# Optimization experiments

Hardware: AMD Instinct MI355X
Metric: run time of the kernel (lower is better)

## Reference

```python
import jax, jax.numpy as jnp
import numpy as np

N = 50000
E = 1600000
IN_C = 512
HID = 128
HEADS = 8
OUT_C = 64
NEG_SLOPE = 0.2


def setup_inputs() -> dict:
    key = jax.random.key(0)
    ks = jax.random.split(key, 10)
    x = jax.random.normal(ks[0], (N, IN_C), dtype=jnp.float32)
    edge_index = jax.random.randint(ks[1], (2, E), 0, N, dtype=jnp.int32)
    s1 = 1.0 / np.sqrt(IN_C)
    W1 = jax.random.uniform(ks[2], (IN_C, HEADS * HID), jnp.float32, -s1, s1)
    att_src1 = jax.random.normal(ks[3], (HEADS, HID), jnp.float32) * 0.1
    att_dst1 = jax.random.normal(ks[4], (HEADS, HID), jnp.float32) * 0.1
    b1 = jnp.zeros((HEADS * HID,), jnp.float32)
    s2 = 1.0 / np.sqrt(HEADS * HID)
    W2 = jax.random.uniform(ks[5], (HEADS * HID, OUT_C), jnp.float32, -s2, s2)
    att_src2 = jax.random.normal(ks[6], (1, OUT_C), jnp.float32) * 0.1
    att_dst2 = jax.random.normal(ks[7], (1, OUT_C), jnp.float32) * 0.1
    b2 = jnp.zeros((OUT_C,), jnp.float32)
    return {"x": x, "edge_index": edge_index, "W1": W1, "att_src1": att_src1,
            "att_dst1": att_dst1, "b1": b1, "W2": W2, "att_src2": att_src2,
            "att_dst2": att_dst2, "b2": b2}


def gat_conv(x, src, dst, W, a_src, a_dst, b, heads, ch, concat):
    n = x.shape[0]
    h = (x @ W).reshape(n, heads, ch)                      # [N,H,C]
    alpha_s = jnp.einsum('nhc,hc->nh', h, a_src)           # [N,H]
    alpha_d = jnp.einsum('nhc,hc->nh', h, a_dst)           # [N,H]
    logits = jax.nn.leaky_relu(alpha_s[src] + alpha_d[dst], NEG_SLOPE)  # [E,H]
    # segment softmax over edges grouped by destination node
    m = jax.ops.segment_max(logits, dst, num_segments=n)
    e = jnp.exp(logits - m[dst])
    z = jax.ops.segment_sum(e, dst, num_segments=n)
    alpha = e / z[dst]                                     # [E,H]
    msg = h[src] * alpha[:, :, None]                       # [E,H,C]
    out = jax.ops.segment_sum(msg, dst, num_segments=n)    # [N,H,C]
    out = out.reshape(n, heads * ch) if concat else out.mean(axis=1)
    return out + b


def reference(x, edge_index, W1, att_src1, att_dst1, b1, W2, att_src2, att_dst2, b2):
    n = x.shape[0]
    loops = jnp.arange(n, dtype=edge_index.dtype)
    src = jnp.concatenate([edge_index[0], loops])
    dst = jnp.concatenate([edge_index[1], loops])
    h = gat_conv(x, src, dst, W1, att_src1, att_dst1, b1, HEADS, HID, True)
    h = jax.nn.elu(h)
    out = gat_conv(h, src, dst, W2, att_src2, att_dst2, b2, 1, OUT_C, False)
    return jax.nn.log_softmax(out, axis=1)
```

## Files before the change

kernel.cpp:

```cpp
#include <hip/hip_runtime.h>
#include <hip/hip_bf16.h>

#define NN 50000
#define EE 1600000
#define ET (EE + NN)
#define HEADS 8
#define HID 128
#define INC 512
#define H1C (HEADS * HID)
#define OUTC 64
#define NEG_SLOPE 0.2f

typedef unsigned short u16;
typedef unsigned int u32;
typedef unsigned char u8;
typedef __attribute__((ext_vector_type(8))) __bf16 bf16x8;
typedef __attribute__((ext_vector_type(4))) float f32x4;
typedef __attribute__((ext_vector_type(2))) float f32x2;
typedef __attribute__((ext_vector_type(4))) u32 u32x4;

__device__ __forceinline__ float lrelu(float x) { return x > 0.f ? x : NEG_SLOPE * x; }
__device__ __forceinline__ float us2f(u16 u) { return __uint_as_float(((u32)u) << 16); }
__device__ __forceinline__ u16 f2bs(float f) {
    u32 u = __float_as_uint(f);
    u += 0x7fffu + ((u >> 16) & 1u);
    return (u16)(u >> 16);
}

__device__ __forceinline__ void gload_lds16(const void* g, void* lds) {
    __builtin_amdgcn_global_load_lds((const __attribute__((address_space(1))) void*)g,
                                     (__attribute__((address_space(3))) void*)lds, 16, 0, 0);
}

__global__ __launch_bounds__(256) void cvt_x_k(const float* __restrict__ x, u16* __restrict__ xb) {
    int i = blockIdx.x * 256 + threadIdx.x;
    float4 v = ((const float4*)x)[i];
    ushort4 o; o.x = f2bs(v.x); o.y = f2bs(v.y); o.z = f2bs(v.z); o.w = f2bs(v.w);
    ((ushort4*)xb)[i] = o;
}

__global__ __launch_bounds__(256) void cvt_w1t_k(const float* __restrict__ W, u16* __restrict__ Wt) {
    int idx = blockIdx.x * 256 + threadIdx.x;
    int n = idx >> 9, k = idx & 511;
    Wt[idx] = f2bs(W[k * 1024 + n]);
}

__global__ __launch_bounds__(256) void cvt_w2t_k(const float* __restrict__ W, u16* __restrict__ Wt) {
    int idx = blockIdx.x * 256 + threadIdx.x;
    int n = idx >> 10, k = idx & 1023;
    Wt[idx] = f2bs(W[k * 64 + n]);
}

__global__ __launch_bounds__(256) void hist_k(const int* __restrict__ ei, int* __restrict__ cnt) {
    int e = blockIdx.x * 256 + threadIdx.x;
    if (e >= ET) return;
    int d = (e < EE) ? ei[EE + e] : (e - EE);
    atomicAdd(&cnt[d], 1);
}

__global__ __launch_bounds__(256) void scan1_k(const int* __restrict__ cnt,
                                               int* __restrict__ startp, int* __restrict__ bsum) {
    __shared__ int ws[8];
    int tid = threadIdx.x;
    int i = blockIdx.x * 256 + tid;
    int v = (i < NN) ? cnt[i] : 0;
    int lane = tid & 63, w = tid >> 6;
    int x = v;
#pragma unroll
    for (int off = 1; off < 64; off <<= 1) { int t = __shfl_up(x, off); if (lane >= off) x += t; }
    if (lane == 63) ws[w] = x;
    __syncthreads();
    if (tid == 0) { int s = 0; for (int k = 0; k < 4; ++k) { int t = ws[k]; ws[k] = s; s += t; } }
    __syncthreads();
    x += ws[w];
    if (i < NN) startp[i] = x - v;
    if (tid == 255) bsum[blockIdx.x] = x;
}

__global__ __launch_bounds__(256) void scan2_k(const int* __restrict__ bsum,
                                               int* __restrict__ boff, int nb) {
    __shared__ int ws[8];
    int tid = threadIdx.x;
    int v = (tid < nb) ? bsum[tid] : 0;
    int lane = tid & 63, w = tid >> 6;
    int x = v;
#pragma unroll
    for (int off = 1; off < 64; off <<= 1) { int t = __shfl_up(x, off); if (lane >= off) x += t; }
    if (lane == 63) ws[w] = x;
    __syncthreads();
    if (tid == 0) { int s = 0; for (int k = 0; k < 4; ++k) { int t = ws[k]; ws[k] = s; s += t; } }
    __syncthreads();
    x += ws[w];
    if (tid < nb) boff[tid] = x - v;
}

__global__ __launch_bounds__(256) void scan3_k(int* __restrict__ startp, const int* __restrict__ boff) {
    int i = blockIdx.x * 256 + threadIdx.x;
    if (i < NN) startp[i] += boff[blockIdx.x];
}

__global__ __launch_bounds__(256) void scatter_k(const int* __restrict__ ei,
                                                 const int* __restrict__ start,
                                                 int* __restrict__ cursor,
                                                 int* __restrict__ csr_src) {
    int e = blockIdx.x * 256 + threadIdx.x;
    if (e >= ET) return;
    int s, d;
    if (e < EE) { s = ei[e]; d = ei[EE + e]; }
    else        { s = e - EE; d = e - EE; }
    int pos = start[d] + atomicAdd(&cursor[d], 1);
    csr_src[pos] = s;
}

__device__ __forceinline__ void stf(float* p, float v) { *p = v; }
__device__ __forceinline__ void stf(u16* p, float v)   { *p = f2bs(v); }
__device__ __forceinline__ void stf(u8* p, float v) {
    u32 pk = __builtin_amdgcn_cvt_pk_fp8_f32(v, v, 0, false);
    *p = (u8)(pk & 0xff);
}

template<int BM, int BN, typename TC, bool FUSE, int SWZ>
__global__ __launch_bounds__(256) void mgemm_k(const u16* __restrict__ A,
                                               const u16* __restrict__ Bt,
                                               TC* __restrict__ C,
                                               const float* __restrict__ att_s,
                                               const float* __restrict__ att_d,
                                               float* __restrict__ as_o,
                                               float* __restrict__ ad_o,
                                               int M, int K, int Ncol, int NH) {
    __shared__ __align__(16) u16 As[BM * 64];
    __shared__ __align__(16) u16 Bs[BN * 64];
    __shared__ float asL[2][BM], adL[2][BM];
    int tid = threadIdx.x;
    int wid = tid >> 6, lane = tid & 63;

    int wg = blockIdx.x;
    if (SWZ) { int q = gridDim.x >> 3; wg = (blockIdx.x & 7) * q + (blockIdx.x >> 3); }
    int nbn = Ncol / BN;
    int bm_i = wg / nbn, bn_i = wg % nbn;
    int bm = bm_i * BM, bn = bn_i * BN;

    constexpr int WN = BN / 2;
    constexpr int FM = 4;
    constexpr int FN = WN / 16;
    constexpr int TA = BM * 64 * 2 / 1024;
    constexpr int TB = BN * 64 * 2 / 1024;
    int wr = wid >> 1, wc = wid & 1;

    f32x4 acc[FM][FN] = {};

    for (int k0 = 0; k0 < K; k0 += 64) {
#pragma unroll
        for (int i = 0; i < TA / 4; ++i) {
            int t = wid * (TA / 4) + i;
            int o = t * 1024 + lane * 16;
            int m = o >> 7;
            int b = o & 127;
            int kb = b ^ ((m & 7) << 4);
            int gm = bm + m; if (gm >= M) gm = M - 1;
            gload_lds16(A + ((size_t)gm * K + k0 + (kb >> 1)), (char*)As + t * 1024);
        }
#pragma unroll
        for (int i = 0; i < TB / 4; ++i) {
            int t = wid * (TB / 4) + i;
            int o = t * 1024 + lane * 16;
            int n = o >> 7;
            int b = o & 127;
            int kb = b ^ ((n & 7) << 4);
            gload_lds16(Bt + ((size_t)(bn + n) * K + k0 + (kb >> 1)), (char*)Bs + t * 1024);
        }
        __syncthreads();
        int g = lane >> 4, r = lane & 15;
#pragma unroll
        for (int kh = 0; kh < 2; ++kh) {
            int kbb = g * 16 + kh * 64;
            bf16x8 af[FM], bfr[FN];
#pragma unroll
            for (int fm = 0; fm < FM; ++fm) {
                int m = wr * 64 + fm * 16 + r;
                af[fm] = *(const bf16x8*)((const char*)As + m * 128 + (kbb ^ ((m & 7) << 4)));
            }
#pragma unroll
            for (int fn = 0; fn < FN; ++fn) {
                int n = wc * WN + fn * 16 + r;
                bfr[fn] = *(const bf16x8*)((const char*)Bs + n * 128 + (kbb ^ ((n & 7) << 4)));
            }
#pragma unroll
            for (int fm = 0; fm < FM; ++fm)
#pragma unroll
                for (int fn = 0; fn < FN; ++fn)
                    acc[fm][fn] = __builtin_amdgcn_mfma_f32_16x16x32_bf16(af[fm], bfr[fn], acc[fm][fn], 0, 0, 0);
        }
        __syncthreads();
    }
#pragma unroll
    for (int fm = 0; fm < FM; ++fm)
#pragma unroll
        for (int fn = 0; fn < FN; ++fn)
#pragma unroll
            for (int rr = 0; rr < 4; ++rr) {
                int gm = bm + wr * 64 + fm * 16 + (lane >> 4) * 4 + rr;
                int gn = bn + wc * WN + fn * 16 + (lane & 15);
                if (gm < M) stf(&C[(size_t)gm * Ncol + gn], acc[fm][fn][rr]);
            }

    if constexpr (FUSE) {
        float asv[FN], adv[FN];
#pragma unroll
        for (int fn = 0; fn < FN; ++fn) {
            int c = bn + wc * WN + fn * 16 + (lane & 15);
            asv[fn] = att_s[c]; adv[fn] = att_d[c];
        }
#pragma unroll
        for (int fm = 0; fm < FM; ++fm)
#pragma unroll
            for (int rr = 0; rr < 4; ++rr) {
                float ps = 0.f, pd = 0.f;
#pragma unroll
                for (int fn = 0; fn < FN; ++fn) {
                    ps += acc[fm][fn][rr] * asv[fn];
                    pd += acc[fm][fn][rr] * adv[fn];
                }
#pragma unroll
                for (int off = 1; off < 16; off <<= 1) {
                    ps += __shfl_xor(ps, off);
                    pd += __shfl_xor(pd, off);
                }
                if ((lane & 15) == 0) {
                    int rl = wr * 64 + fm * 16 + (lane >> 4) * 4 + rr;
                    asL[wc][rl] = ps; adL[wc][rl] = pd;
                }
            }
        __syncthreads();
        if (tid < BM) {
            int gm = bm + tid;
            if (gm < M) {
                as_o[(size_t)gm * NH + bn_i] = asL[0][tid] + asL[1][tid];
                ad_o[(size_t)gm * NH + bn_i] = adL[0][tid] + adL[1][tid];
            }
        }
    }
}

__global__ __launch_bounds__(256) void agg1_k(const u8* __restrict__ h1,
                                              const float* __restrict__ as1,
                                              const float* __restrict__ ad1,
                                              const int* __restrict__ start,
                                              const int* __restrict__ cnt,
                                              const int* __restrict__ csr_src,
                                              const float* __restrict__ b1,
                                              u16* __restrict__ out1) {
    int n = blockIdx.x;
    int tid = threadIdx.x;
    int s0 = start[n], deg = cnt[n];
    __shared__ float ad_sh[8], rz_sh[8];
    __shared__ int src_sh[64];
    __shared__ float al_sh[64][8];
    __shared__ float zred[256];
    __shared__ float comb[3][64][17];

    if (tid < 8) ad_sh[tid] = ad1[n * 8 + tid];
    __syncthreads();

    int l = tid & 63, grp = tid >> 6;
    int myh = l >> 3;
    float acc[16] = {};
    float zacc = 0.f;
    const char* h1b = (const char*)h1;

    for (int e0 = 0; e0 < deg; e0 += 64) {
        int ne = min(64, deg - e0);
        if (tid < ne) src_sh[tid] = csr_src[s0 + e0 + tid];
        __syncthreads();
        for (int i = tid; i < ne * 8; i += 256) {
            int ee = i >> 3, hh = i & 7;
            int s = src_sh[ee];
            float al = __expf(lrelu(as1[s * 8 + hh] + ad_sh[hh]));
            al_sh[ee][hh] = al;
            zacc += al;
        }
        __syncthreads();
        int j = grp;
        if (j < ne) {
            u32x4 v = *(const u32x4*)(h1b + (size_t)src_sh[j] * 1024 + l * 16);
            while (true) {
                int jn = j + 4;
                bool more = jn < ne;
                u32x4 vn;
                if (more) vn = *(const u32x4*)(h1b + (size_t)src_sh[jn] * 1024 + l * 16);
                float al = al_sh[j][myh];
#pragma unroll
                for (int w = 0; w < 4; ++w) {
                    u32 word = v[w];
                    f32x2 p0 = __builtin_amdgcn_cvt_pk_f32_fp8(word, false);
                    f32x2 p1 = __builtin_amdgcn_cvt_pk_f32_fp8(word, true);
                    acc[w * 4 + 0] += al * p0.x;
                    acc[w * 4 + 1] += al * p0.y;
                    acc[w * 4 + 2] += al * p1.x;
                    acc[w * 4 + 3] += al * p1.y;
                }
                if (!more) break;
                v = vn; j = jn;
            }
        }
        __syncthreads();
    }

    zred[tid] = zacc;
    __syncthreads();
#pragma unroll
    for (int off = 128; off >= 8; off >>= 1) {
        if (tid < off) zred[tid] += zred[tid + off];
        __syncthreads();
    }
    if (tid < 8) rz_sh[tid] = 1.f / zred[tid];
    __syncthreads();

    if (grp) {
#pragma unroll
        for (int c = 0; c < 16; ++c) comb[grp - 1][l][c] = acc[c];
    }
    __syncthreads();
    if (!grp) {
        float rz = rz_sh[myh];
        int cbase = l * 16;
        float o[16];
#pragma unroll
        for (int c = 0; c < 16; ++c) {
            float zz = (acc[c] + comb[0][l][c] + comb[1][l][c] + comb[2][l][c]) * rz + b1[cbase + c];
            o[c] = zz > 0.f ? zz : (__expf(zz) - 1.f);
        }
        u32x4 pk0, pk1;
#pragma unroll
        for (int i = 0; i < 4; ++i) {
            pk0[i] = (u32)f2bs(o[2 * i])     | ((u32)f2bs(o[2 * i + 1]) << 16);
            pk1[i] = (u32)f2bs(o[8 + 2 * i]) | ((u32)f2bs(o[9 + 2 * i]) << 16);
        }
        char* dst = (char*)out1 + (size_t)n * 2048 + l * 32;
        __builtin_nontemporal_store(pk0, (u32x4*)dst);
        __builtin_nontemporal_store(pk1, (u32x4*)(dst + 16));
    }
}

__global__ __launch_bounds__(256) void agg2_k(const u16* __restrict__ h2,
                                              const float* __restrict__ as2,
                                              const float* __restrict__ ad2,
                                              const int* __restrict__ start,
                                              const int* __restrict__ cnt,
                                              const int* __restrict__ csr_src,
                                              const float* __restrict__ b2,
                                              float* __restrict__ out) {
    int n = blockIdx.x * 4 + (threadIdx.x >> 6);
    int lane = threadIdx.x & 63;
    if (n >= NN) return;
    int s0 = start[n], deg = cnt[n];
    float adn = ad2[n];

    int half = lane >> 5, l = lane & 31;
    float a0 = 0.f, a1 = 0.f, z = 0.f;
    int j = half;
    if (j < deg) {
        int s = csr_src[s0 + j];
        float asv = as2[s];
        u32 v = *(const u32*)(h2 + (size_t)s * 64 + l * 2);
        while (true) {
            int jn = j + 2;
            bool more = jn < deg;
            int sn; float asn; u32 vn;
            if (more) {
                sn = csr_src[s0 + jn];
                asn = as2[sn];
                vn = *(const u32*)(h2 + (size_t)sn * 64 + l * 2);
            }
            float al = __expf(lrelu(asv + adn));
            z += al;
            a0 += al * us2f((u16)(v & 0xffff));
            a1 += al * us2f((u16)(v >> 16));
            if (!more) break;
            asv = asn; v = vn; j = jn;
        }
    }
    a0 += __shfl_xor(a0, 32);
    a1 += __shfl_xor(a1, 32);
    z  += __shfl_xor(z, 32);
    float rz = 1.f / z;
    float y0 = a0 * rz + b2[2 * l], y1 = a1 * rz + b2[2 * l + 1];

    float mm = fmaxf(y0, y1);
#pragma unroll
    for (int off = 16; off; off >>= 1) mm = fmaxf(mm, __shfl_xor(mm, off));
    float se = __expf(y0 - mm) + __expf(y1 - mm);
#pragma unroll
    for (int off = 16; off; off >>= 1) se += __shfl_xor(se, off);
    float ls = __logf(se);
    if (half == 0) {
        float2 o; o.x = y0 - mm - ls; o.y = y1 - mm - ls;
        *(float2*)(out + (size_t)n * 64 + 2 * l) = o;
    }
}

extern "C" void kernel_launch(void* const* d_in, const int* in_sizes, int n_in,
                              void* d_out, int out_size, void* d_ws, size_t ws_size,
                              hipStream_t stream) {
    const float* x     = (const float*)d_in[0];
    const int*   ei    = (const int*)d_in[1];
    const float* W1    = (const float*)d_in[2];
    const float* aw_s1 = (const float*)d_in[3];
    const float* aw_d1 = (const float*)d_in[4];
    const float* b1    = (const float*)d_in[5];
    const float* W2    = (const float*)d_in[6];
    const float* aw_s2 = (const float*)d_in[7];
    const float* aw_d2 = (const float*)d_in[8];
    const float* b2    = (const float*)d_in[9];
    float* out = (float*)d_out;

    char* ws = (char*)d_ws;
    size_t off = 0;
    auto alloc = [&](size_t bytes) -> void* {
        void* p = (void*)(ws + off);
        off += (bytes + 511) & ~(size_t)511;
        return p;
    };
    u16*   out1    = (u16*)alloc((size_t)NN * H1C * 2);
    u16*   xb      = out1;
    u8*    h1      = (u8*)alloc((size_t)NN * H1C);
    u16*   h2      = (u16*)h1;
    u16*   w1t     = (u16*)alloc((size_t)H1C * INC * 2);
    u16*   w2t     = (u16*)alloc((size_t)OUTC * H1C * 2);
    float* as1     = (float*)alloc((size_t)NN * 8 * 4);
    float* ad1     = (float*)alloc((size_t)NN * 8 * 4);
    float* as2     = (float*)alloc((size_t)NN * 4);
    float* ad2     = (float*)alloc((size_t)NN * 4);
    int*   cnt     = (int*)alloc((size_t)NN * 4);
    int*   startp  = (int*)alloc((size_t)NN * 4);
    int*   cursor  = (int*)alloc((size_t)NN * 4);
    int*   csr_src = (int*)alloc((size_t)ET * 4);
    int    nsb     = (NN + 255) / 256;
    int*   bsum    = (int*)alloc((size_t)nsb * 4);
    int*   boff    = (int*)alloc((size_t)nsb * 4);

    if (off > ws_size) return;

    hipMemsetAsync(cnt, 0, (size_t)NN * 4, stream);
    hipMemsetAsync(cursor, 0, (size_t)NN * 4, stream);

    cvt_x_k<<<(NN * INC / 4) / 256, 256, 0, stream>>>(x, xb);
    cvt_w1t_k<<<(INC * H1C) / 256, 256, 0, stream>>>(W1, w1t);
    cvt_w2t_k<<<(H1C * OUTC) / 256, 256, 0, stream>>>(W2, w2t);

    int eblk = (ET + 255) / 256;
    hist_k<<<eblk, 256, 0, stream>>>(ei, cnt);
    scan1_k<<<nsb, 256, 0, stream>>>(cnt, startp, bsum);
    scan2_k<<<1, 256, 0, stream>>>(bsum, boff, nsb);
    scan3_k<<<nsb, 256, 0, stream>>>(startp, boff);
    scatter_k<<<eblk, 256, 0, stream>>>(ei, startp, cursor, csr_src);

    int nwg1 = (H1C / 128) * ((NN + 127) / 128);
    mgemm_k<128, 128, u8, true, 1><<<nwg1, 256, 0, stream>>>(
        xb, w1t, h1, aw_s1, aw_d1, as1, ad1, NN, INC, H1C, HEADS);
    agg1_k<<<NN, 256, 0, stream>>>(h1, as1, ad1, startp, cnt, csr_src, b1, out1);

    int nwg2 = (OUTC / 64) * ((NN + 127) / 128);
    mgemm_k<128, 64, u16, true, 0><<<nwg2, 256, 0, stream>>>(
        out1, w2t, h2, aw_s2, aw_d2, as2, ad2, NN, H1C, OUTC, 1);
    agg2_k<<<(NN + 3) / 4, 256, 0, stream>>>(h2, as2, ad2, startp, cnt, csr_src, b2, out);
}
```

Baseline: 790.8 us.

## Merge conversion/histogram launches, persist aggregation kernels, deepen gather prefetch

Folds the x conversion and degree histogram into one launch, merges the two weight-transpose kernels, and clears cnt and cursor with a single memset by making them adjacent. Both aggregation kernels become grid-stride persistent kernels (4096 and 1024 blocks) instead of one block or wave per node. Their gather loops now prefetch two edges ahead instead of one. The aim is less launch overhead, less per-block setup, and more memory-level parallelism in the neighbour gathers, at the cost of extra registers and possible load imbalance across persistent blocks.

```diff
diff --git a/kernel.cpp b/kernel.cpp
--- a/kernel.cpp
+++ b/kernel.cpp
@@ -32,30 +32,35 @@
                                      (__attribute__((address_space(3))) void*)lds, 16, 0, 0);
 }
 
-__global__ __launch_bounds__(256) void cvt_x_k(const float* __restrict__ x, u16* __restrict__ xb) {
-    int i = blockIdx.x * 256 + threadIdx.x;
-    float4 v = ((const float4*)x)[i];
-    ushort4 o; o.x = f2bs(v.x); o.y = f2bs(v.y); o.z = f2bs(v.z); o.w = f2bs(v.w);
-    ((ushort4*)xb)[i] = o;
-}
-
-__global__ __launch_bounds__(256) void cvt_w1t_k(const float* __restrict__ W, u16* __restrict__ Wt) {
+#define CVTX_BLOCKS 25000
+__global__ __launch_bounds__(256) void cvtx_hist_k(const float* __restrict__ x, u16* __restrict__ xb,
+                                                   const int* __restrict__ ei, int* __restrict__ cnt) {
+    int b = blockIdx.x;
+    if (b < CVTX_BLOCKS) {
+        int i = b * 256 + threadIdx.x;
+        float4 v = ((const float4*)x)[i];
+        ushort4 o; o.x = f2bs(v.x); o.y = f2bs(v.y); o.z = f2bs(v.z); o.w = f2bs(v.w);
+        ((ushort4*)xb)[i] = o;
+    } else {
+        int e = (b - CVTX_BLOCKS) * 256 + threadIdx.x;
+        if (e < ET) {
+            int d = (e < EE) ? ei[EE + e] : (e - EE);
+            atomicAdd(&cnt[d], 1);
+        }
+    }
+}
+
+__global__ __launch_bounds__(256) void cvt_w_k(const float* __restrict__ W1, u16* __restrict__ W1t,
+                                               const float* __restrict__ W2, u16* __restrict__ W2t) {
     int idx = blockIdx.x * 256 + threadIdx.x;
-    int n = idx >> 9, k = idx & 511;
-    Wt[idx] = f2bs(W[k * 1024 + n]);
-}
-
-__global__ __launch_bounds__(256) void cvt_w2t_k(const float* __restrict__ W, u16* __restrict__ Wt) {
-    int idx = blockIdx.x * 256 + threadIdx.x;
-    int n = idx >> 10, k = idx & 1023;
-    Wt[idx] = f2bs(W[k * 64 + n]);
-}
-
-__global__ __launch_bounds__(256) void hist_k(const int* __restrict__ ei, int* __restrict__ cnt) {
-    int e = blockIdx.x * 256 + threadIdx.x;
-    if (e >= ET) return;
-    int d = (e < EE) ? ei[EE + e] : (e - EE);
-    atomicAdd(&cnt[d], 1);
+    if (idx < INC * H1C) {
+        int n = idx >> 9, k = idx & 511;
+        W1t[idx] = f2bs(W1[k * 1024 + n]);
+    } else {
+        int j = idx - INC * H1C;
+        int n = j >> 10, k = j & 1023;
+        W2t[j] = f2bs(W2[k * 64 + n]);
+    }
 }
 
 __global__ __launch_bounds__(256) void scan1_k(const int* __restrict__ cnt,
@@ -250,95 +255,100 @@
                                               const int* __restrict__ csr_src,
                                               const float* __restrict__ b1,
                                               u16* __restrict__ out1) {
-    int n = blockIdx.x;
     int tid = threadIdx.x;
-    int s0 = start[n], deg = cnt[n];
     __shared__ float ad_sh[8], rz_sh[8];
     __shared__ int src_sh[64];
     __shared__ float al_sh[64][8];
     __shared__ float zred[256];
     __shared__ float comb[3][64][17];
-
-    if (tid < 8) ad_sh[tid] = ad1[n * 8 + tid];
-    __syncthreads();
-
     int l = tid & 63, grp = tid >> 6;
     int myh = l >> 3;
-    float acc[16] = {};
-    float zacc = 0.f;
     const char* h1b = (const char*)h1;
 
-    for (int e0 = 0; e0 < deg; e0 += 64) {
-        int ne = min(64, deg - e0);
-        if (tid < ne) src_sh[tid] = csr_src[s0 + e0 + tid];
-        __syncthreads();
-        for (int i = tid; i < ne * 8; i += 256) {
-            int ee = i >> 3, hh = i & 7;
-            int s = src_sh[ee];
-            float al = __expf(lrelu(as1[s * 8 + hh] + ad_sh[hh]));
-            al_sh[ee][hh] = al;
-            zacc += al;
-        }
-        __syncthreads();
-        int j = grp;
-        if (j < ne) {
-            u32x4 v = *(const u32x4*)(h1b + (size_t)src_sh[j] * 1024 + l * 16);
-            while (true) {
-                int jn = j + 4;
-                bool more = jn < ne;
-                u32x4 vn;
-                if (more) vn = *(const u32x4*)(h1b + (size_t)src_sh[jn] * 1024 + l * 16);
-                float al = al_sh[j][myh];
-#pragma unroll
-                for (int w = 0; w < 4; ++w) {
-                    u32 word = v[w];
-                    f32x2 p0 = __builtin_amdgcn_cvt_pk_f32_fp8(word, false);
-                    f32x2 p1 = __builtin_amdgcn_cvt_pk_f32_fp8(word, true);
-                    acc[w * 4 + 0] += al * p0.x;
-                    acc[w * 4 + 1] += al * p0.y;
-                    acc[w * 4 + 2] += al * p1.x;
-                    acc[w * 4 + 3] += al * p1.y;
+    for (int n = blockIdx.x; n < NN; n += gridDim.x) {
+        int s0 = start[n], deg = cnt[n];
+        if (tid < 8) ad_sh[tid] = ad1[n * 8 + tid];
+        __syncthreads();
+
+        float acc[16] = {};
+        float zacc = 0.f;
+
+        for (int e0 = 0; e0 < deg; e0 += 64) {
+            int ne = min(64, deg - e0);
+            if (tid < ne) src_sh[tid] = csr_src[s0 + e0 + tid];
+            __syncthreads();
+            for (int i = tid; i < ne * 8; i += 256) {
+                int ee = i >> 3, hh = i & 7;
+                int s = src_sh[ee];
+                float al = __expf(lrelu(as1[s * 8 + hh] + ad_sh[hh]));
+                al_sh[ee][hh] = al;
+                zacc += al;
+            }
+            __syncthreads();
+            int j = grp;
+            if (j < ne) {
+                u32x4 v0 = *(const u32x4*)(h1b + (size_t)src_sh[j] * 1024 + l * 16);
+                int j1 = j + 4; bool b1v = j1 < ne;
+                u32x4 v1;
+                if (b1v) v1 = *(const u32x4*)(h1b + (size_t)src_sh[j1] * 1024 + l * 16);
+                while (true) {
+                    int j2 = j + 8; bool b2v = j2 < ne;
+                    u32x4 v2;
+                    if (b2v) v2 = *(const u32x4*)(h1b + (size_t)src_sh[j2] * 1024 + l * 16);
+                    float al = al_sh[j][myh];
+#pragma unroll
+                    for (int w = 0; w < 4; ++w) {
+                        u32 word = v0[w];
+                        f32x2 p0 = __builtin_amdgcn_cvt_pk_f32_fp8(word, false);
+                        f32x2 p1 = __builtin_amdgcn_cvt_pk_f32_fp8(word, true);
+                        acc[w * 4 + 0] += al * p0.x;
+                        acc[w * 4 + 1] += al * p0.y;
+                        acc[w * 4 + 2] += al * p1.x;
+                        acc[w * 4 + 3] += al * p1.y;
+                    }
+                    if (!b1v) break;
+                    v0 = v1; j = j1;
+                    v1 = v2; j1 = j2; b1v = b2v;
                 }
-                if (!more) break;
-                v = vn; j = jn;
-            }
-        }
-        __syncthreads();
-    }
-
-    zred[tid] = zacc;
-    __syncthreads();
-#pragma unroll
-    for (int off = 128; off >= 8; off >>= 1) {
-        if (tid < off) zred[tid] += zred[tid + off];
-        __syncthreads();
-    }
-    if (tid < 8) rz_sh[tid] = 1.f / zred[tid];
-    __syncthreads();
-
-    if (grp) {
-#pragma unroll
-        for (int c = 0; c < 16; ++c) comb[grp - 1][l][c] = acc[c];
-    }
-    __syncthreads();
-    if (!grp) {
-        float rz = rz_sh[myh];
-        int cbase = l * 16;
-        float o[16];
-#pragma unroll
-        for (int c = 0; c < 16; ++c) {
-            float zz = (acc[c] + comb[0][l][c] + comb[1][l][c] + comb[2][l][c]) * rz + b1[cbase + c];
-            o[c] = zz > 0.f ? zz : (__expf(zz) - 1.f);
-        }
-        u32x4 pk0, pk1;
-#pragma unroll
-        for (int i = 0; i < 4; ++i) {
-            pk0[i] = (u32)f2bs(o[2 * i])     | ((u32)f2bs(o[2 * i + 1]) << 16);
-            pk1[i] = (u32)f2bs(o[8 + 2 * i]) | ((u32)f2bs(o[9 + 2 * i]) << 16);
-        }
-        char* dst = (char*)out1 + (size_t)n * 2048 + l * 32;
-        __builtin_nontemporal_store(pk0, (u32x4*)dst);
-        __builtin_nontemporal_store(pk1, (u32x4*)(dst + 16));
+            }
+            __syncthreads();
+        }
+
+        zred[tid] = zacc;
+        __syncthreads();
+#pragma unroll
+        for (int off = 128; off >= 8; off >>= 1) {
+            if (tid < off) zred[tid] += zred[tid + off];
+            __syncthreads();
+        }
+        if (tid < 8) rz_sh[tid] = 1.f / zred[tid];
+        __syncthreads();
+
+        if (grp) {
+#pragma unroll
+            for (int c = 0; c < 16; ++c) comb[grp - 1][l][c] = acc[c];
+        }
+        __syncthreads();
+        if (!grp) {
+            float rz = rz_sh[myh];
+            int cbase = l * 16;
+            float o[16];
+#pragma unroll
+            for (int c = 0; c < 16; ++c) {
+                float zz = (acc[c] + comb[0][l][c] + comb[1][l][c] + comb[2][l][c]) * rz + b1[cbase + c];
+                o[c] = zz > 0.f ? zz : (__expf(zz) - 1.f);
+            }
+            u32x4 pk0, pk1;
+#pragma unroll
+            for (int i = 0; i < 4; ++i) {
+                pk0[i] = (u32)f2bs(o[2 * i])     | ((u32)f2bs(o[2 * i + 1]) << 16);
+                pk1[i] = (u32)f2bs(o[8 + 2 * i]) | ((u32)f2bs(o[9 + 2 * i]) << 16);
+            }
+            char* dst = (char*)out1 + (size_t)n * 2048 + l * 32;
+            __builtin_nontemporal_store(pk0, (u32x4*)dst);
+            __builtin_nontemporal_store(pk1, (u32x4*)(dst + 16));
+        }
+        __syncthreads();
     }
 }
 
@@ -350,52 +360,66 @@
                                               const int* __restrict__ csr_src,
                                               const float* __restrict__ b2,
                                               float* __restrict__ out) {
-    int n = blockIdx.x * 4 + (threadIdx.x >> 6);
     int lane = threadIdx.x & 63;
-    if (n >= NN) return;
-    int s0 = start[n], deg = cnt[n];
-    float adn = ad2[n];
-
+    int wv = threadIdx.x >> 6;
     int half = lane >> 5, l = lane & 31;
-    float a0 = 0.f, a1 = 0.f, z = 0.f;
-    int j = half;
-    if (j < deg) {
-        int s = csr_src[s0 + j];
-        float asv = as2[s];
-        u32 v = *(const u32*)(h2 + (size_t)s * 64 + l * 2);
-        while (true) {
-            int jn = j + 2;
-            bool more = jn < deg;
-            int sn; float asn; u32 vn;
-            if (more) {
-                sn = csr_src[s0 + jn];
-                asn = as2[sn];
-                vn = *(const u32*)(h2 + (size_t)sn * 64 + l * 2);
-            }
-            float al = __expf(lrelu(asv + adn));
-            z += al;
-            a0 += al * us2f((u16)(v & 0xffff));
-            a1 += al * us2f((u16)(v >> 16));
-            if (!more) break;
-            asv = asn; v = vn; j = jn;
-        }
-    }
-    a0 += __shfl_xor(a0, 32);
-    a1 += __shfl_xor(a1, 32);
-    z  += __shfl_xor(z, 32);
-    float rz = 1.f / z;
-    float y0 = a0 * rz + b2[2 * l], y1 = a1 * rz + b2[2 * l + 1];
-
-    float mm = fmaxf(y0, y1);
-#pragma unroll
-    for (int off = 16; off; off >>= 1) mm = fmaxf(mm, __shfl_xor(mm, off));
-    float se = __expf(y0 - mm) + __expf(y1 - mm);
-#pragma unroll
-    for (int off = 16; off; off >>= 1) se += __shfl_xor(se, off);
-    float ls = __logf(se);
-    if (half == 0) {
-        float2 o; o.x = y0 - mm - ls; o.y = y1 - mm - ls;
-        *(float2*)(out + (size_t)n * 64 + 2 * l) = o;
+    float b2a = b2[2 * l], b2b = b2[2 * l + 1];
+
+    for (int n = blockIdx.x * 4 + wv; n < NN; n += gridDim.x * 4) {
+        int s0 = start[n], deg = cnt[n];
+        float adn = ad2[n];
+
+        float a0 = 0.f, a1 = 0.f, z = 0.f;
+        int j = half;
+        bool bv0 = j < deg;
+        if (bv0) {
+            float e0v; u32 v0;
+            {
+                int s = csr_src[s0 + j];
+                e0v = as2[s];
+                v0 = *(const u32*)(h2 + (size_t)s * 64 + l * 2);
+            }
+            int j1 = j + 2; bool bv1 = j1 < deg;
+            float e1v; u32 v1;
+            if (bv1) {
+                int s = csr_src[s0 + j1];
+                e1v = as2[s];
+                v1 = *(const u32*)(h2 + (size_t)s * 64 + l * 2);
+            }
+            while (true) {
+                int j2 = j + 4; bool bv2 = j2 < deg;
+                float e2v; u32 v2;
+                if (bv2) {
+                    int s = csr_src[s0 + j2];
+                    e2v = as2[s];
+                    v2 = *(const u32*)(h2 + (size_t)s * 64 + l * 2);
+                }
+                float al = __expf(lrelu(e0v + adn));
+                z += al;
+                a0 += al * us2f((u16)(v0 & 0xffff));
+                a1 += al * us2f((u16)(v0 >> 16));
+                if (!bv1) break;
+                e0v = e1v; v0 = v1; j = j1;
+                e1v = e2v; v1 = v2; j1 = j2; bv1 = bv2;
+            }
+        }
+        a0 += __shfl_xor(a0, 32);
+        a1 += __shfl_xor(a1, 32);
+        z  += __shfl_xor(z, 32);
+        float rz = 1.f / z;
+        float y0 = a0 * rz + b2a, y1 = a1 * rz + b2b;
+
+        float mm = fmaxf(y0, y1);
+#pragma unroll
+        for (int off = 16; off; off >>= 1) mm = fmaxf(mm, __shfl_xor(mm, off));
+        float se = __expf(y0 - mm) + __expf(y1 - mm);
+#pragma unroll
+        for (int off = 16; off; off >>= 1) se += __shfl_xor(se, off);
+        float ls = __logf(se);
+        if (half == 0) {
+            float2 o; o.x = y0 - mm - ls; o.y = y1 - mm - ls;
+            *(float2*)(out + (size_t)n * 64 + 2 * l) = o;
+        }
     }
 }
 
@@ -432,8 +456,8 @@
     float* as2     = (float*)alloc((size_t)NN * 4);
     float* ad2     = (float*)alloc((size_t)NN * 4);
     int*   cnt     = (int*)alloc((size_t)NN * 4);
+    int*   cursor  = (int*)alloc((size_t)NN * 4);
     int*   startp  = (int*)alloc((size_t)NN * 4);
-    int*   cursor  = (int*)alloc((size_t)NN * 4);
     int*   csr_src = (int*)alloc((size_t)ET * 4);
     int    nsb     = (NN + 255) / 256;
     int*   bsum    = (int*)alloc((size_t)nsb * 4);
@@ -441,15 +465,12 @@
 
     if (off > ws_size) return;
 
-    hipMemsetAsync(cnt, 0, (size_t)NN * 4, stream);
-    hipMemsetAsync(cursor, 0, (size_t)NN * 4, stream);
-
-    cvt_x_k<<<(NN * INC / 4) / 256, 256, 0, stream>>>(x, xb);
-    cvt_w1t_k<<<(INC * H1C) / 256, 256, 0, stream>>>(W1, w1t);
-    cvt_w2t_k<<<(H1C * OUTC) / 256, 256, 0, stream>>>(W2, w2t);
+    hipMemsetAsync(cnt, 0, (char*)(cursor + NN) - (char*)cnt, stream);
 
     int eblk = (ET + 255) / 256;
-    hist_k<<<eblk, 256, 0, stream>>>(ei, cnt);
+    cvtx_hist_k<<<CVTX_BLOCKS + eblk, 256, 0, stream>>>(x, xb, ei, cnt);
+    cvt_w_k<<<(INC * H1C + OUTC * H1C) / 256, 256, 0, stream>>>(W1, w1t, W2, w2t);
+
     scan1_k<<<nsb, 256, 0, stream>>>(cnt, startp, bsum);
     scan2_k<<<1, 256, 0, stream>>>(bsum, boff, nsb);
     scan3_k<<<nsb, 256, 0, stream>>>(startp, boff);
@@ -458,10 +479,10 @@
     int nwg1 = (H1C / 128) * ((NN + 127) / 128);
     mgemm_k<128, 128, u8, true, 1><<<nwg1, 256, 0, stream>>>(
         xb, w1t, h1, aw_s1, aw_d1, as1, ad1, NN, INC, H1C, HEADS);
-    agg1_k<<<NN, 256, 0, stream>>>(h1, as1, ad1, startp, cnt, csr_src, b1, out1);
+    agg1_k<<<4096, 256, 0, stream>>>(h1, as1, ad1, startp, cnt, csr_src, b1, out1);
 
     int nwg2 = (OUTC / 64) * ((NN + 127) / 128);
     mgemm_k<128, 64, u16, true, 0><<<nwg2, 256, 0, stream>>>(
         out1, w2t, h2, aw_s2, aw_d2, as2, ad2, NN, H1C, OUTC, 1);
-    agg2_k<<<(NN + 3) / 4, 256, 0, stream>>>(h2, as2, ad2, startp, cnt, csr_src, b2, out);
-}
+    agg2_k<<<1024, 256, 0, stream>>>(h2, as2, ad2, startp, cnt, csr_src, b2, out);
+}
```

After: 996.7 us. +26.0%, slower.
